# Performance work log

Measured on AMD Instinct MI355X. Metric: run time of the kernel, lower is better.

## Reference

```python
import jax, jax.numpy as jnp
import numpy as np

T, B, IN, H, OUT = 2048, 512, 27, 64, 26
EPS = 1e-5
DROP = 0.1


def setup_inputs() -> dict:
    key = jax.random.key(0)
    ks = jax.random.split(key, 11)
    s = 1.0 / np.sqrt(H)
    u = lambda k, shape: jax.random.uniform(k, shape, jnp.float32, -s, s)
    return {
        "obscure_word": jax.random.normal(ks[0], (T, B, IN), jnp.float32),
        "prev_guess": jax.random.uniform(ks[1], (T, OUT), jnp.float32),
        "W_ih": u(ks[2], (4 * H, IN)),
        "W_hh": u(ks[3], (4 * H, H)),
        "b_ih": u(ks[4], (4 * H,)),
        "b_hh": u(ks[5], (4 * H,)),
        "gamma": jnp.ones((H,), jnp.float32),
        "beta": jnp.zeros((H,), jnp.float32),
        "W_fc": u(ks[6], (OUT, H + OUT)),
        "b_fc": u(ks[7], (OUT,)),
        # LockedDropout mask: sampled once, reused every timestep, pre-scaled by 1/(1-p)
        "drop_mask": (jax.random.uniform(ks[8], (B, H)) < (1.0 - DROP)).astype(jnp.float32) / (1.0 - DROP),
    }


def reference(obscure_word, prev_guess, W_ih, W_hh, b_ih, b_hh, gamma, beta, W_fc, b_fc, drop_mask):
    h0 = jnp.zeros((B, H), obscure_word.dtype)
    c0 = jnp.zeros((B, H), obscure_word.dtype)

    def step(carry, inputs):
        h, c = carry
        x_t, pg_t = inputs  # [B, IN], [OUT]
        gates = x_t @ W_ih.T + b_ih + h @ W_hh.T + b_hh  # [B, 4H]
        i, f, g, o = jnp.split(gates, 4, axis=1)
        i = jax.nn.sigmoid(i)
        f = jax.nn.sigmoid(f)
        g = jnp.tanh(g)
        o = jax.nn.sigmoid(o)
        c_new = f * c + i * g
        h_new = o * jnp.tanh(c_new)
        # BatchNorm1d (training mode: per-timestep batch stats, biased var)
        mean = jnp.mean(h_new, axis=0)
        var = jnp.mean((h_new - mean) ** 2, axis=0)
        hb = (h_new - mean) * jax.lax.rsqrt(var + EPS) * gamma + beta
        # LockedDropout (same mask every timestep)
        hd = hb * drop_mask
        # MaxPool1d over batch dim -> [H]
        pooled = jnp.max(hd, axis=0)
        out = jnp.concatenate([pooled, pg_t])  # [H+OUT]
        y = out @ W_fc.T + b_fc  # [OUT]
        return (h_new, c_new), y

    _, ys = jax.lax.scan(step, (h0, c0), (obscure_word, prev_guess))
    return ys[:, None, :]  # [T, 1, OUT]
```

## Files before the change

### kernel.cpp

```cpp
#include <hip/hip_runtime.h>
#include <hip/hip_bf16.h>

#define TT   2048
#define BB   512
#define IN_  27
#define HH   64
#define NG   256
#define OUTD 26
#define EPSV 1e-5f

__device__ __forceinline__ float bcastf(float v, int lane) {
    return __int_as_float(__builtin_amdgcn_readlane(__float_as_int(v), lane));
}

__device__ __forceinline__ float sigm(float x) {
    return 1.0f / (1.0f + __expf(-x));
}

__device__ __forceinline__ float tanh_fast(float x) {
    float e = __expf(-2.0f * fabsf(x));
    float r = (1.0f - e) / (1.0f + e);
    return copysignf(r, x);
}

__global__ __launch_bounds__(256, 2) void lstm_seq(
    const float* __restrict__ x,
    const float* __restrict__ W_ih,
    const float* __restrict__ W_hh,
    const float* __restrict__ b_ih,
    const float* __restrict__ b_hh,
    float* __restrict__ h_all,
    float* __restrict__ state,
    int t0, int tc, int first)
{
    const int b = blockIdx.x;
    const int j = threadIdx.x;
    const int q = j >> 6;
    const int l = j & 63;

    float wi[IN_];
#pragma unroll
    for (int k = 0; k < IN_; ++k) wi[k] = W_ih[j * IN_ + k];
    float wh[HH];
#pragma unroll
    for (int k = 0; k < HH; ++k) wh[k] = W_hh[j * HH + k];
    const float bias = b_ih[j] + b_hh[j];

    float hv, cv;
    if (first) {
        hv = 0.0f; cv = 0.0f;
    } else {
        hv = state[b * HH + l];
        cv = state[BB * HH + b * HH + l];
    }

    __shared__ float acts[2][NG];

    for (int tl = 0; tl < tc; ++tl) {
        const int t = t0 + tl;

        float xv = 0.0f;
        if (l < IN_) xv = x[((size_t)t * BB + b) * IN_ + l];

        float a0 = bias, a1 = 0.0f, a2 = 0.0f, a3 = 0.0f;
#pragma unroll
        for (int k = 0; k < HH; k += 4) {
            a0 = fmaf(bcastf(hv, k + 0), wh[k + 0], a0);
            a1 = fmaf(bcastf(hv, k + 1), wh[k + 1], a1);
            a2 = fmaf(bcastf(hv, k + 2), wh[k + 2], a2);
            a3 = fmaf(bcastf(hv, k + 3), wh[k + 3], a3);
        }
#pragma unroll
        for (int k = 0; k < 24; k += 4) {
            a0 = fmaf(bcastf(xv, k + 0), wi[k + 0], a0);
            a1 = fmaf(bcastf(xv, k + 1), wi[k + 1], a1);
            a2 = fmaf(bcastf(xv, k + 2), wi[k + 2], a2);
            a3 = fmaf(bcastf(xv, k + 3), wi[k + 3], a3);
        }
        a0 = fmaf(bcastf(xv, 24), wi[24], a0);
        a1 = fmaf(bcastf(xv, 25), wi[25], a1);
        a2 = fmaf(bcastf(xv, 26), wi[26], a2);
        const float acc = (a0 + a1) + (a2 + a3);

        const float av = (q == 2) ? tanh_fast(acc) : sigm(acc);

        acts[tl & 1][j] = av;
        __syncthreads();

        const float gi = acts[tl & 1][l];
        const float gf = acts[tl & 1][HH + l];
        const float gg = acts[tl & 1][2 * HH + l];
        const float go = acts[tl & 1][3 * HH + l];

        const float cn = fmaf(gf, cv, gi * gg);
        const float hn = go * tanh_fast(cn);
        cv = cn;
        hv = hn;

        if (q == 0) h_all[((size_t)tl * BB + b) * HH + l] = hn;
    }

    if (q == 0) {
        state[b * HH + l] = hv;
        state[BB * HH + b * HH + l] = cv;
    }
}

__global__ __launch_bounds__(256, 2) void bn_pool_fc(
    const float* __restrict__ h_all,
    const float* __restrict__ gamma,
    const float* __restrict__ beta,
    const float* __restrict__ dmask,
    const float* __restrict__ pg,
    const float* __restrict__ W_fc,
    const float* __restrict__ b_fc,
    float* __restrict__ y,
    int t0, int tc)
{
    const int tl = blockIdx.x;
    const int t = t0 + tl;
    const int tid = threadIdx.x;
    const int g = tid >> 6;
    const int hcol = tid & 63;
    const float* hp = h_all + (size_t)tl * BB * HH;

    __shared__ float s_a[4][HH];
    __shared__ float s_b[4][HH];
    __shared__ float s_scale[HH];
    __shared__ float s_shift[HH];
    __shared__ float s_pool[HH];

    float sum = 0.0f, sq = 0.0f;
    for (int bb = g; bb < BB; bb += 4) {
        const float v = hp[bb * HH + hcol];
        sum += v;
        sq = fmaf(v, v, sq);
    }
    s_a[g][hcol] = sum;
    s_b[g][hcol] = sq;
    __syncthreads();

    if (tid < HH) {
        const float s  = (s_a[0][tid] + s_a[1][tid]) + (s_a[2][tid] + s_a[3][tid]);
        const float q2 = (s_b[0][tid] + s_b[1][tid]) + (s_b[2][tid] + s_b[3][tid]);
        const float mean = s * (1.0f / BB);
        const float var  = q2 * (1.0f / BB) - mean * mean;
        const float rs = rsqrtf(var + EPSV);
        const float sc = rs * gamma[tid];
        s_scale[tid] = sc;
        s_shift[tid] = beta[tid] - mean * sc;
    }
    __syncthreads();

    const float sc = s_scale[hcol];
    const float sh = s_shift[hcol];
    float m = -3.0e38f;
    for (int bb = g; bb < BB; bb += 4) {
        const float v = hp[bb * HH + hcol];
        const float hd = fmaf(v, sc, sh) * dmask[bb * HH + hcol];
        m = fmaxf(m, hd);
    }
    s_a[g][hcol] = m;
    __syncthreads();
    if (tid < HH) {
        s_pool[tid] = fmaxf(fmaxf(s_a[0][tid], s_a[1][tid]),
                            fmaxf(s_a[2][tid], s_a[3][tid]));
    }
    __syncthreads();

    if (tid < OUTD) {
        float acc = b_fc[tid];
        const float* w = W_fc + tid * (HH + OUTD);
#pragma unroll
        for (int k = 0; k < HH; ++k) acc = fmaf(w[k], s_pool[k], acc);
#pragma unroll
        for (int k = 0; k < OUTD; ++k) acc = fmaf(w[HH + k], pg[t * OUTD + k], acc);
        y[t * OUTD + tid] = acc;
    }
}

extern "C" void kernel_launch(void* const* d_in, const int* in_sizes, int n_in,
                              void* d_out, int out_size, void* d_ws, size_t ws_size,
                              hipStream_t stream)
{
    const float* x     = (const float*)d_in[0];
    const float* pg    = (const float*)d_in[1];
    const float* W_ih  = (const float*)d_in[2];
    const float* W_hh  = (const float*)d_in[3];
    const float* b_ih  = (const float*)d_in[4];
    const float* b_hh  = (const float*)d_in[5];
    const float* gamma = (const float*)d_in[6];
    const float* beta  = (const float*)d_in[7];
    const float* W_fc  = (const float*)d_in[8];
    const float* b_fc  = (const float*)d_in[9];
    const float* dmask = (const float*)d_in[10];
    float* y = (float*)d_out;

    const size_t state_bytes = 2ull * BB * HH * sizeof(float);
    const size_t per_t = (size_t)BB * HH * sizeof(float);
    size_t avail = (ws_size > state_bytes) ? (ws_size - state_bytes) : 0;
    int chunkT = (int)(avail / per_t);
    if (chunkT > TT) chunkT = TT;
    if (chunkT < 1) chunkT = 1;

    float* h_all = (float*)d_ws;
    float* state = (float*)((char*)d_ws + (size_t)chunkT * per_t);

    int first = 1;
    for (int t0 = 0; t0 < TT; t0 += chunkT) {
        int tc = TT - t0;
        if (tc > chunkT) tc = chunkT;
        lstm_seq<<<BB, 256, 0, stream>>>(x, W_ih, W_hh, b_ih, b_hh,
                                         h_all, state, t0, tc, first);
        bn_pool_fc<<<tc, 256, 0, stream>>>(h_all, gamma, beta, dmask, pg,
                                           W_fc, b_fc, y, t0, tc);
        first = 0;
    }
}
```

Before: 2.235 ms.

## Precompute input gate projections in a parallel kernel and broadcast h via LDS

Moves the x·W_ih + bias projection out of the sequential recurrence into a separate fully parallel kernel that writes gate_x to workspace. The recurrent kernel then only does the h·W_hh product. It reads h from shared memory as float4 instead of using readlane broadcasts, and the W_hh registers are pinned with empty asm. This shortens the per-step serial critical path, at the cost of extra global traffic for gate_x (B*4H floats per step), a second barrier per step, and smaller time chunks because the workspace must now also hold gate_x.

```diff
diff --git a/kernel.cpp b/kernel.cpp
--- a/kernel.cpp
+++ b/kernel.cpp
@@ -9,10 +9,6 @@
 #define OUTD 26
 #define EPSV 1e-5f
 
-__device__ __forceinline__ float bcastf(float v, int lane) {
-    return __int_as_float(__builtin_amdgcn_readlane(__float_as_int(v), lane));
-}
-
 __device__ __forceinline__ float sigm(float x) {
     return 1.0f / (1.0f + __expf(-x));
 }
@@ -23,85 +19,117 @@
     return copysignf(r, x);
 }
 
-__global__ __launch_bounds__(256, 2) void lstm_seq(
+#define PIN16(a,b,c,d,e,f,g,h,i,jj,k,ll,m,n,o,p) \
+    asm volatile("" : "+v"(a),"+v"(b),"+v"(c),"+v"(d),"+v"(e),"+v"(f),"+v"(g),"+v"(h), \
+                      "+v"(i),"+v"(jj),"+v"(k),"+v"(ll),"+v"(m),"+v"(n),"+v"(o),"+v"(p));
+
+__global__ __launch_bounds__(256) void gate_x_pre(
     const float* __restrict__ x,
     const float* __restrict__ W_ih,
-    const float* __restrict__ W_hh,
     const float* __restrict__ b_ih,
     const float* __restrict__ b_hh,
+    float* __restrict__ gate_x,
+    int t0, int tc)
+{
+    const int j  = threadIdx.x;
+    const int tl = blockIdx.x;
+    const int bg = blockIdx.y;
+    const float bias = b_ih[j] + b_hh[j];
+    const float* wr = W_ih + (size_t)j * IN_;
+
+#pragma unroll
+    for (int bb8 = 0; bb8 < 8; ++bb8) {
+        const int b = bg * 8 + bb8;
+        const float* xr = x + ((size_t)(t0 + tl) * BB + b) * IN_;
+        float acc = bias;
+#pragma unroll
+        for (int k = 0; k < IN_; ++k) acc = fmaf(xr[k], wr[k], acc);
+        gate_x[((size_t)tl * BB + b) * NG + j] = acc;
+    }
+}
+
+__global__ __launch_bounds__(256, 2) void lstm_seq(
+    const float* __restrict__ gate_x,
+    const float* __restrict__ W_hh,
     float* __restrict__ h_all,
     float* __restrict__ state,
-    int t0, int tc, int first)
+    int tc, int first)
 {
     const int b = blockIdx.x;
     const int j = threadIdx.x;
     const int q = j >> 6;
     const int l = j & 63;
 
-    float wi[IN_];
-#pragma unroll
-    for (int k = 0; k < IN_; ++k) wi[k] = W_ih[j * IN_ + k];
-    float wh[HH];
-#pragma unroll
-    for (int k = 0; k < HH; ++k) wh[k] = W_hh[j * HH + k];
-    const float bias = b_ih[j] + b_hh[j];
-
-    float hv, cv;
-    if (first) {
-        hv = 0.0f; cv = 0.0f;
-    } else {
-        hv = state[b * HH + l];
-        cv = state[BB * HH + b * HH + l];
-    }
-
-    __shared__ float acts[2][NG];
+    const float4* whv = (const float4*)W_hh + (size_t)j * 16;
+    float4 v0 = whv[0],  v1 = whv[1],  v2 = whv[2],  v3 = whv[3];
+    float4 v4 = whv[4],  v5 = whv[5],  v6 = whv[6],  v7 = whv[7];
+    float4 v8 = whv[8],  v9 = whv[9],  v10 = whv[10], v11 = whv[11];
+    float4 v12 = whv[12], v13 = whv[13], v14 = whv[14], v15 = whv[15];
+#define UNP(m, V) float wh##m##0=(V).x, wh##m##1=(V).y, wh##m##2=(V).z, wh##m##3=(V).w;
+    UNP(0,v0) UNP(1,v1) UNP(2,v2) UNP(3,v3) UNP(4,v4) UNP(5,v5) UNP(6,v6) UNP(7,v7)
+    UNP(8,v8) UNP(9,v9) UNP(10,v10) UNP(11,v11) UNP(12,v12) UNP(13,v13) UNP(14,v14) UNP(15,v15)
+#undef UNP
+    PIN16(wh00,wh01,wh02,wh03, wh10,wh11,wh12,wh13, wh20,wh21,wh22,wh23, wh30,wh31,wh32,wh33)
+    PIN16(wh40,wh41,wh42,wh43, wh50,wh51,wh52,wh53, wh60,wh61,wh62,wh63, wh70,wh71,wh72,wh73)
+    PIN16(wh80,wh81,wh82,wh83, wh90,wh91,wh92,wh93, wh100,wh101,wh102,wh103, wh110,wh111,wh112,wh113)
+    PIN16(wh120,wh121,wh122,wh123, wh130,wh131,wh132,wh133, wh140,wh141,wh142,wh143, wh150,wh151,wh152,wh153)
+
+    float cv, hcur;
+    if (first) { cv = 0.0f; hcur = 0.0f; }
+    else {
+        hcur = state[b * HH + l];
+        cv   = state[BB * HH + b * HH + l];
+    }
+
+    __shared__ float  acts[NG];
+    __shared__ float4 hbuf[16];
+
+    if (q == 0) ((float*)hbuf)[l] = hcur;
+    __syncthreads();
+
+    const float* gxp = gate_x + (size_t)b * NG + j;
+    float gx = *gxp;
 
     for (int tl = 0; tl < tc; ++tl) {
-        const int t = t0 + tl;
-
-        float xv = 0.0f;
-        if (l < IN_) xv = x[((size_t)t * BB + b) * IN_ + l];
-
-        float a0 = bias, a1 = 0.0f, a2 = 0.0f, a3 = 0.0f;
-#pragma unroll
-        for (int k = 0; k < HH; k += 4) {
-            a0 = fmaf(bcastf(hv, k + 0), wh[k + 0], a0);
-            a1 = fmaf(bcastf(hv, k + 1), wh[k + 1], a1);
-            a2 = fmaf(bcastf(hv, k + 2), wh[k + 2], a2);
-            a3 = fmaf(bcastf(hv, k + 3), wh[k + 3], a3);
-        }
-#pragma unroll
-        for (int k = 0; k < 24; k += 4) {
-            a0 = fmaf(bcastf(xv, k + 0), wi[k + 0], a0);
-            a1 = fmaf(bcastf(xv, k + 1), wi[k + 1], a1);
-            a2 = fmaf(bcastf(xv, k + 2), wi[k + 2], a2);
-            a3 = fmaf(bcastf(xv, k + 3), wi[k + 3], a3);
-        }
-        a0 = fmaf(bcastf(xv, 24), wi[24], a0);
-        a1 = fmaf(bcastf(xv, 25), wi[25], a1);
-        a2 = fmaf(bcastf(xv, 26), wi[26], a2);
+        const float* gxn = gxp + ((tl + 1 < tc) ? (size_t)BB * NG : 0);
+        const float gx_n = *gxn;
+
+        float a0 = gx, a1 = 0.0f, a2 = 0.0f, a3 = 0.0f;
+#define HD(m) { float4 h4 = hbuf[m]; \
+        a0 = fmaf(h4.x, wh##m##0, a0); \
+        a1 = fmaf(h4.y, wh##m##1, a1); \
+        a2 = fmaf(h4.z, wh##m##2, a2); \
+        a3 = fmaf(h4.w, wh##m##3, a3); }
+        HD(0) HD(1) HD(2) HD(3) HD(4) HD(5) HD(6) HD(7)
+        HD(8) HD(9) HD(10) HD(11) HD(12) HD(13) HD(14) HD(15)
+#undef HD
         const float acc = (a0 + a1) + (a2 + a3);
 
         const float av = (q == 2) ? tanh_fast(acc) : sigm(acc);
-
-        acts[tl & 1][j] = av;
+        acts[j] = av;
         __syncthreads();
 
-        const float gi = acts[tl & 1][l];
-        const float gf = acts[tl & 1][HH + l];
-        const float gg = acts[tl & 1][2 * HH + l];
-        const float go = acts[tl & 1][3 * HH + l];
+        const float gi = acts[l];
+        const float gf = acts[HH + l];
+        const float gg = acts[2 * HH + l];
+        const float go = acts[3 * HH + l];
 
         const float cn = fmaf(gf, cv, gi * gg);
         const float hn = go * tanh_fast(cn);
         cv = cn;
-        hv = hn;
-
-        if (q == 0) h_all[((size_t)tl * BB + b) * HH + l] = hn;
+        hcur = hn;
+
+        if (q == 0) {
+            ((float*)hbuf)[l] = hn;
+            h_all[((size_t)tl * BB + b) * HH + l] = hn;
+        }
+        __syncthreads();
+        gx = gx_n;
+        gxp += (size_t)BB * NG;
     }
 
     if (q == 0) {
-        state[b * HH + l] = hv;
+        state[b * HH + l] = hcur;
         state[BB * HH + b * HH + l] = cv;
     }
 }
@@ -197,21 +225,23 @@
     float* y = (float*)d_out;
 
     const size_t state_bytes = 2ull * BB * HH * sizeof(float);
-    const size_t per_t = (size_t)BB * HH * sizeof(float);
+    const size_t per_t = (size_t)BB * HH * sizeof(float) + (size_t)BB * NG * sizeof(float);
     size_t avail = (ws_size > state_bytes) ? (ws_size - state_bytes) : 0;
     int chunkT = (int)(avail / per_t);
     if (chunkT > TT) chunkT = TT;
     if (chunkT < 1) chunkT = 1;
 
-    float* h_all = (float*)d_ws;
-    float* state = (float*)((char*)d_ws + (size_t)chunkT * per_t);
+    float* h_all  = (float*)d_ws;
+    float* gate_x = h_all + (size_t)chunkT * BB * HH;
+    float* state  = gate_x + (size_t)chunkT * BB * NG;
 
     int first = 1;
     for (int t0 = 0; t0 < TT; t0 += chunkT) {
         int tc = TT - t0;
         if (tc > chunkT) tc = chunkT;
-        lstm_seq<<<BB, 256, 0, stream>>>(x, W_ih, W_hh, b_ih, b_hh,
-                                         h_all, state, t0, tc, first);
+        gate_x_pre<<<dim3(tc, BB / 8), 256, 0, stream>>>(x, W_ih, b_ih, b_hh,
+                                                         gate_x, t0, tc);
+        lstm_seq<<<BB, 256, 0, stream>>>(gate_x, W_hh, h_all, state, tc, first);
         bn_pool_fc<<<tc, 256, 0, stream>>>(h_all, gamma, beta, dmask, pg,
                                            W_fc, b_fc, y, t0, tc);
         first = 0;
```

Measured after the change: 6.857 ms. +206.8%, slower.
